# Kernel optimization log

Measured on AMD Instinct MI355X. Metric: run time of the kernel, lower is better.

## Reference

```python
import jax, jax.numpy as jnp
import numpy as np

B, N, C = 4, 2048, 1024
H = 16
D = C // H

def setup_inputs() -> dict:
    key = jax.random.key(0)
    k1, k2, k3 = jax.random.split(key, 3)
    x = jax.random.normal(k1, (B, N, C), dtype=jnp.float32)
    qkv_w = jax.random.normal(k2, (3 * C, C), dtype=jnp.float32) * (1.0 / np.sqrt(C))
    qkv_b = jax.random.normal(k3, (3 * C,), dtype=jnp.float32) * 0.02
    return {"x": x, "qkv_w": qkv_w, "qkv_b": qkv_b}

def reference(x, qkv_w, qkv_b):
    b, n, c = x.shape
    # torch Linear: x @ W^T + b
    qkv = x @ qkv_w.T + qkv_b                      # [B,N,3C]
    qkv = qkv.reshape(b, n, 3, H, D)
    qkv = jnp.transpose(qkv, (2, 0, 3, 1, 4))       # [3,B,H,N,D]
    q, k, v = qkv[0], qkv[1], qkv[2]
    attn = jnp.einsum('bhnd,bhmd->bhnm', q, k) / jnp.sqrt(jnp.asarray(D, x.dtype))
    attn = jax.nn.softmax(attn, axis=-1)
    out = jnp.einsum('bhnm,bhmd->bhnd', attn, v)    # [B,H,N,D]
    out = jnp.transpose(out, (0, 2, 1, 3)).reshape(b, n, c)
    return out
```

## Files before the change

### kernel.cpp

```cpp
#include <hip/hip_runtime.h>
#include <hip/hip_bf16.h>

typedef __attribute__((ext_vector_type(8))) short short8;
typedef __attribute__((ext_vector_type(4))) float f32x4;
typedef __attribute__((ext_vector_type(4))) unsigned int u32x4;
typedef unsigned short u16;
typedef unsigned int u32;

typedef u32 __attribute__((address_space(1))) as1_u32;
typedef u32 __attribute__((address_space(3))) as3_u32;

#define NB 4
#define SEQ 2048
#define CH 1024
#define NH 16
#define HD 64
#define M_TOT (NB*SEQ)
#define N_TOT (3*CH)
#define K_TOT CH
#define SCL 0.18033688f

#define MFMA16(a,b,c) __builtin_amdgcn_mfma_f32_16x16x32_bf16((a),(b),(c),0,0,0)

__device__ __forceinline__ u16 f2bf(float f) {
    union { float f; u32 u; } v; v.f = f;
    u32 u = v.u;
    return (u16)((u + 0x7fffu + ((u >> 16) & 1u)) >> 16);
}

__device__ __forceinline__ u32 pkbf2(float a, float b) {
    union { __hip_bfloat162 h; u32 u; } x;
    x.h = __float22bfloat162_rn(float2{a, b});
    return x.u;
}

__global__ void cvt_bf16_kernel(const float* __restrict__ x, u16* __restrict__ xb, int nx8,
                                const float* __restrict__ w, u16* __restrict__ wb, int nw8) {
    int i = blockIdx.x * 256 + threadIdx.x;
    const float* src; u16* dst; int idx;
    if (i < nx8) { src = x; dst = xb; idx = i; }
    else { idx = i - nx8; if (idx >= nw8) return; src = w; dst = wb; }
    const float4* s4 = (const float4*)src;
    float4 a = s4[2*idx], b = s4[2*idx+1];
    u32x4 r;
    r[0] = pkbf2(a.x, a.y); r[1] = pkbf2(a.z, a.w);
    r[2] = pkbf2(b.x, b.y); r[3] = pkbf2(b.z, b.w);
    *(u32x4*)(dst + (size_t)idx*8) = r;
}

__global__ __launch_bounds__(256) void qkv_gemm_kernel(
        const u16* __restrict__ A, const u16* __restrict__ W,
        const float* __restrict__ bias,
        u16* __restrict__ qw, u16* __restrict__ kw, u16* __restrict__ vtw)
{
    __shared__ u16 As[128*32];
    __shared__ u16 Bs[128*32];
    const int t = threadIdx.x;
    const int wave = t >> 6;
    const int lane = t & 63;
    const int l15 = lane & 15, lhi = lane >> 4;
    const int wr = wave >> 1, wc = wave & 1;
    const int xcd = blockIdx.x & 7;
    const int idx = blockIdx.x >> 3;
    const int bm = xcd * 8 + (idx & 7);
    const int bn = idx >> 3;

    f32x4 acc[4][4] = {};

    const int arow = t >> 2;
    const int acol = (t & 3) * 8;
    const u16* gA = A + (size_t)(bm*128 + arow)*K_TOT + acol;
    const u16* gB = W + (size_t)(bn*128 + arow)*K_TOT + acol;

    for (int k0 = 0; k0 < K_TOT; k0 += 32) {
        #pragma unroll
        for (int i = 0; i < 2; ++i) {
            __builtin_amdgcn_global_load_lds(
                (const as1_u32*)(gA + (size_t)i*64*K_TOT + k0),
                (as3_u32*)(As + i*2048 + wave*512), 16, 0, 0);
            __builtin_amdgcn_global_load_lds(
                (const as1_u32*)(gB + (size_t)i*64*K_TOT + k0),
                (as3_u32*)(Bs + i*2048 + wave*512), 16, 0, 0);
        }
        __syncthreads();
        short8 af[4], bfr[4];
        #pragma unroll
        for (int m = 0; m < 4; ++m)
            af[m] = *(const short8*)(As + (wr*64 + m*16 + l15)*32 + lhi*8);
        #pragma unroll
        for (int n = 0; n < 4; ++n)
            bfr[n] = *(const short8*)(Bs + (wc*64 + n*16 + l15)*32 + lhi*8);
        #pragma unroll
        for (int m = 0; m < 4; ++m)
            #pragma unroll
            for (int n = 0; n < 4; ++n)
                acc[m][n] = MFMA16(af[m], bfr[n], acc[m][n]);
        __syncthreads();
    }

    const int colbase = bn*128 + wc*64;
    const int which = colbase >> 10;
    float bv[4]; int hh[4], dd[4];
    #pragma unroll
    for (int n = 0; n < 4; ++n) {
        int cg = colbase + n*16 + l15;
        bv[n] = bias[cg];
        int hd = cg & 1023;
        hh[n] = hd >> 6; dd[n] = hd & 63;
    }
    #pragma unroll
    for (int m = 0; m < 4; ++m) {
        int rowg = bm*128 + wr*64 + m*16 + lhi*4;
        #pragma unroll
        for (int j = 0; j < 4; ++j) {
            int rg = rowg + j;
            int b = rg >> 11, nseq = rg & 2047;
            #pragma unroll
            for (int n = 0; n < 4; ++n) {
                float val = acc[m][n][j] + bv[n];
                size_t bhn = (size_t)(b*NH + hh[n]);
                if (which == 0) {
                    qw[(bhn*SEQ + nseq)*HD + dd[n]] = f2bf(val * SCL);
                } else if (which == 1) {
                    kw[(bhn*SEQ + nseq)*HD + dd[n]] = f2bf(val);
                } else {
                    vtw[(bhn*HD + dd[n])*SEQ + nseq] = f2bf(val);
                }
            }
        }
    }
}

__global__ __launch_bounds__(256, 2) void attn_kernel(
        const u16* __restrict__ qw, const u16* __restrict__ kw,
        const u16* __restrict__ vtw, float* __restrict__ out)
{
    __shared__ u16 Ksh[3][64*64];
    __shared__ u16 Vsh[3][64*64];
    const int t = threadIdx.x;
    const int wave = t >> 6, lane = t & 63;
    const int l15 = lane & 15, lhi = lane >> 4;
    const int bh = blockIdx.x & 63;
    const int b = bh >> 4, h = bh & 15;
    const int q0 = (blockIdx.x >> 6) * 256 + wave * 64;

    const u16* Q  = qw  + (size_t)bh * SEQ * HD;
    const u16* Kg = kw  + (size_t)bh * SEQ * HD;
    const u16* Vg = vtw + (size_t)bh * HD * SEQ;

    const int srow = lane >> 3;
    const int scol = ((lane & 7) ^ srow) * 8;

    auto STAGE = [&](int buf, int kv) {
        #pragma unroll
        for (int half = 0; half < 2; ++half) {
            int crow = wave*16 + half*8 + srow;
            int kperm = (crow & 32) | ((crow & 12) << 1)
                      | ((crow & 16) >> 2) | (crow & 3);
            __builtin_amdgcn_global_load_lds(
                (const as1_u32*)(Kg + (size_t)(kv + kperm)*HD + scol),
                (as3_u32*)(&Ksh[buf][(wave*16 + half*8)*64]), 16, 0, 0);
            __builtin_amdgcn_global_load_lds(
                (const as1_u32*)(Vg + (size_t)crow*SEQ + kv + scol),
                (as3_u32*)(&Vsh[buf][(wave*16 + half*8)*64]), 16, 0, 0);
        }
    };

    STAGE(0, 0);
    STAGE(1, 64);

    short8 qf[4][2];
    #pragma unroll
    for (int rf = 0; rf < 4; ++rf)
        #pragma unroll
        for (int ks = 0; ks < 2; ++ks)
            qf[rf][ks] = *(const short8*)(Q + (size_t)(q0 + rf*16 + l15)*HD + ks*32 + lhi*8);

    f32x4 o[4][4] = {};
    float lpart[4] = {0.f, 0.f, 0.f, 0.f};

    const int NT = SEQ / 64;
    int cur = 0;
    for (int tt = 0; tt < NT; ++tt) {
        asm volatile("s_waitcnt vmcnt(4)" ::: "memory");
        __builtin_amdgcn_s_barrier();
        __builtin_amdgcn_sched_barrier(0);

        int nxt = cur + 2; if (nxt >= 3) nxt -= 3;
        int kvn = (tt + 2 < NT) ? (tt + 2) * 64 : 0;
        STAGE(nxt, kvn);

        u32x4 pa[4];
        u32x4 pb[4];
        #pragma unroll
        for (int g = 0; g < 4; ++g) {
            f32x4 stg[4] = {};
            __builtin_amdgcn_s_setprio(1);
            #pragma unroll
            for (int ks = 0; ks < 2; ++ks) {
                short8 kf = *(const short8*)(&Ksh[cur][(g*16 + l15)*64 + ((ks*32 + lhi*8) ^ ((l15 & 7)*8))]);
                #pragma unroll
                for (int rf = 0; rf < 4; ++rf)
                    stg[rf] = MFMA16(kf, qf[rf][ks], stg[rf]);
            }
            __builtin_amdgcn_s_setprio(0);
            #pragma unroll
            for (int rf = 0; rf < 4; ++rf) {
                float p0 = __builtin_amdgcn_exp2f(stg[rf][0]);
                float p1 = __builtin_amdgcn_exp2f(stg[rf][1]);
                float p2 = __builtin_amdgcn_exp2f(stg[rf][2]);
                float p3 = __builtin_amdgcn_exp2f(stg[rf][3]);
                lpart[rf] += (p0 + p1) + (p2 + p3);
                if (g < 2) {
                    pa[rf][(g & 1)*2]     = pkbf2(p0, p1);
                    pa[rf][(g & 1)*2 + 1] = pkbf2(p2, p3);
                } else {
                    pb[rf][(g & 1)*2]     = pkbf2(p0, p1);
                    pb[rf][(g & 1)*2 + 1] = pkbf2(p2, p3);
                }
            }
        }

        __builtin_amdgcn_s_setprio(1);
        #pragma unroll
        for (int ks = 0; ks < 2; ++ks)
            #pragma unroll
            for (int nd = 0; nd < 4; ++nd) {
                short8 vf = *(const short8*)(&Vsh[cur][(nd*16 + l15)*64 + ((ks*32 + lhi*8) ^ ((l15 & 7)*8))]);
                #pragma unroll
                for (int rf = 0; rf < 4; ++rf) {
                    short8 pfrag = __builtin_bit_cast(short8, ks == 0 ? pa[rf] : pb[rf]);
                    o[rf][nd] = MFMA16(pfrag, vf, o[rf][nd]);
                }
            }
        __builtin_amdgcn_s_setprio(0);

        cur = cur + 1; if (cur >= 3) cur -= 3;
    }

    #pragma unroll
    for (int rf = 0; rf < 4; ++rf) {
        float l = lpart[rf];
        l += __shfl_xor(l, 16);
        l += __shfl_xor(l, 32);
        #pragma unroll
        for (int j = 0; j < 4; ++j) {
            float inv = 1.0f / __shfl(l, lhi*4 + j);
            int qrow = q0 + rf*16 + lhi*4 + j;
            float* orow = out + ((size_t)(b*SEQ + qrow))*CH + h*HD;
            #pragma unroll
            for (int nd = 0; nd < 4; ++nd)
                orow[nd*16 + l15] = o[rf][nd][j] * inv;
        }
    }
}

extern "C" void kernel_launch(void* const* d_in, const int* in_sizes, int n_in,
                              void* d_out, int out_size, void* d_ws, size_t ws_size,
                              hipStream_t stream) {
    const float* x    = (const float*)d_in[0];
    const float* w    = (const float*)d_in[1];
    const float* bias = (const float*)d_in[2];
    float* out = (float*)d_out;

    const size_t BHND = (size_t)NB*NH*SEQ*HD;
    u16* qw  = (u16*)d_ws;
    u16* kw  = qw  + BHND;
    u16* vtw = kw  + BHND;
    u16* xbf = vtw + BHND;
    u16* wbf = xbf + (size_t)M_TOT*K_TOT;

    const int nx8 = M_TOT*K_TOT/8;
    const int nw8 = N_TOT*K_TOT/8;
    cvt_bf16_kernel<<<(nx8+nw8+255)/256, 256, 0, stream>>>(x, xbf, nx8, w, wbf, nw8);
    qkv_gemm_kernel<<<(M_TOT/128)*(N_TOT/128), 256, 0, stream>>>(xbf, wbf, bias, qw, kw, vtw);
    attn_kernel<<<(SEQ/256)*NB*NH, 256, 0, stream>>>(qw, kw, vtw, out);
}
```

Baseline: 171.4 us.

## Triple-buffer QKV GEMM LDS tiles with async global_load_lds prefetch

The QKV projection GEMM now keeps three LDS stages for its A and B tiles and prefetches two k-tiles ahead using global_load_lds. A partial vmcnt wait plus a single barrier per iteration replaces the two __syncthreads per iteration, so global loads overlap the MFMA work. This triples LDS use for the GEMM, which may lower occupancy. At the end of the loop it issues redundant dummy loads of tile 0, which are wasted bandwidth.

```diff
diff --git a/kernel.cpp b/kernel.cpp
--- a/kernel.cpp
+++ b/kernel.cpp
@@ -53,8 +53,8 @@
         const float* __restrict__ bias,
         u16* __restrict__ qw, u16* __restrict__ kw, u16* __restrict__ vtw)
 {
-    __shared__ u16 As[128*32];
-    __shared__ u16 Bs[128*32];
+    __shared__ u16 As[3][128*32];
+    __shared__ u16 Bs[3][128*32];
     const int t = threadIdx.x;
     const int wave = t >> 6;
     const int lane = t & 63;
@@ -72,30 +72,46 @@
     const u16* gA = A + (size_t)(bm*128 + arow)*K_TOT + acol;
     const u16* gB = W + (size_t)(bn*128 + arow)*K_TOT + acol;
 
-    for (int k0 = 0; k0 < K_TOT; k0 += 32) {
+    auto STAGE = [&](int s, int kt) {
         #pragma unroll
         for (int i = 0; i < 2; ++i) {
             __builtin_amdgcn_global_load_lds(
-                (const as1_u32*)(gA + (size_t)i*64*K_TOT + k0),
-                (as3_u32*)(As + i*2048 + wave*512), 16, 0, 0);
-            __builtin_amdgcn_global_load_lds(
-                (const as1_u32*)(gB + (size_t)i*64*K_TOT + k0),
-                (as3_u32*)(Bs + i*2048 + wave*512), 16, 0, 0);
-        }
-        __syncthreads();
+                (const as1_u32*)(gA + (size_t)i*64*K_TOT + kt*32),
+                (as3_u32*)(As[s] + i*2048 + wave*512), 16, 0, 0);
+            __builtin_amdgcn_global_load_lds(
+                (const as1_u32*)(gB + (size_t)i*64*K_TOT + kt*32),
+                (as3_u32*)(Bs[s] + i*2048 + wave*512), 16, 0, 0);
+        }
+    };
+
+    STAGE(0, 0);
+    STAGE(1, 1);
+
+    const int NKT = K_TOT / 32;
+    int s = 0;
+    for (int kt = 0; kt < NKT; ++kt) {
+        asm volatile("s_waitcnt vmcnt(4)" ::: "memory");
+        __builtin_amdgcn_s_barrier();
+        __builtin_amdgcn_sched_barrier(0);
+
+        int s2 = (s + 2 >= 3) ? s - 1 : s + 2;
+        int ktn = (kt + 2 < NKT) ? kt + 2 : 0;
+        STAGE(s2, ktn);
+
         short8 af[4], bfr[4];
         #pragma unroll
         for (int m = 0; m < 4; ++m)
-            af[m] = *(const short8*)(As + (wr*64 + m*16 + l15)*32 + lhi*8);
+            af[m] = *(const short8*)(As[s] + (wr*64 + m*16 + l15)*32 + lhi*8);
         #pragma unroll
         for (int n = 0; n < 4; ++n)
-            bfr[n] = *(const short8*)(Bs + (wc*64 + n*16 + l15)*32 + lhi*8);
+            bfr[n] = *(const short8*)(Bs[s] + (wc*64 + n*16 + l15)*32 + lhi*8);
         #pragma unroll
         for (int m = 0; m < 4; ++m)
             #pragma unroll
             for (int n = 0; n < 4; ++n)
                 acc[m][n] = MFMA16(af[m], bfr[n], acc[m][n]);
-        __syncthreads();
+
+        s = (s + 1 >= 3) ? 0 : s + 1;
     }
 
     const int colbase = bn*128 + wc*64;
```

After: 170.0 us. About the same (-0.8%).

## Widen QKV GEMM K-tile to 64 with XOR-swizzled LDS layout

Applied to the files above, without the earlier changes.

The QKV projection GEMM now stages 64-wide K slices per iteration instead of 32, which halves the number of barrier pairs and loop iterations. The LDS tile is stored with an XOR swizzle of 16-byte groups by row, applied on the global source side of the direct-to-LDS loads, so that the MFMA fragment reads avoid bank conflicts. This doubles the LDS footprint per block and adds address arithmetic, and the kernel is still single-buffered.

```diff
diff --git a/kernel.cpp b/kernel.cpp
--- a/kernel.cpp
+++ b/kernel.cpp
@@ -53,8 +53,8 @@
         const float* __restrict__ bias,
         u16* __restrict__ qw, u16* __restrict__ kw, u16* __restrict__ vtw)
 {
-    __shared__ u16 As[128*32];
-    __shared__ u16 Bs[128*32];
+    __shared__ u16 As[128*64];
+    __shared__ u16 Bs[128*64];
     const int t = threadIdx.x;
     const int wave = t >> 6;
     const int lane = t & 63;
@@ -67,34 +67,49 @@
 
     f32x4 acc[4][4] = {};
 
-    const int arow = t >> 2;
-    const int acol = (t & 3) * 8;
-    const u16* gA = A + (size_t)(bm*128 + arow)*K_TOT + acol;
-    const u16* gB = W + (size_t)(bn*128 + arow)*K_TOT + acol;
-
-    for (int k0 = 0; k0 < K_TOT; k0 += 32) {
-        #pragma unroll
-        for (int i = 0; i < 2; ++i) {
-            __builtin_amdgcn_global_load_lds(
-                (const as1_u32*)(gA + (size_t)i*64*K_TOT + k0),
-                (as3_u32*)(As + i*2048 + wave*512), 16, 0, 0);
-            __builtin_amdgcn_global_load_lds(
-                (const as1_u32*)(gB + (size_t)i*64*K_TOT + k0),
-                (as3_u32*)(Bs + i*2048 + wave*512), 16, 0, 0);
+    const int srow = t >> 3;
+    const int sgr  = t & 7;
+
+    const u16* gA = A + (size_t)(bm*128)*K_TOT;
+    const u16* gB = W + (size_t)(bn*128)*K_TOT;
+
+    const int NKT = K_TOT / 64;
+    for (int kt = 0; kt < NKT; ++kt) {
+        #pragma unroll
+        for (int i = 0; i < 4; ++i) {
+            int row = i*32 + srow;
+            int gs = (sgr ^ (row & 7)) * 8;
+            __builtin_amdgcn_global_load_lds(
+                (const as1_u32*)(gA + (size_t)row*K_TOT + kt*64 + gs),
+                (as3_u32*)(As + row*64 + sgr*8), 16, 0, 0);
+            __builtin_amdgcn_global_load_lds(
+                (const as1_u32*)(gB + (size_t)row*K_TOT + kt*64 + gs),
+                (as3_u32*)(Bs + row*64 + sgr*8), 16, 0, 0);
         }
         __syncthreads();
-        short8 af[4], bfr[4];
+
+        short8 af[4][2], bfr[4][2];
+        #pragma unroll
+        for (int m = 0; m < 4; ++m) {
+            int row = wr*64 + m*16 + l15;
+            #pragma unroll
+            for (int kk = 0; kk < 2; ++kk)
+                af[m][kk] = *(const short8*)(&As[row*64 + (((kk*4 + lhi) ^ (row & 7))*8)]);
+        }
+        #pragma unroll
+        for (int n = 0; n < 4; ++n) {
+            int row = wc*64 + n*16 + l15;
+            #pragma unroll
+            for (int kk = 0; kk < 2; ++kk)
+                bfr[n][kk] = *(const short8*)(&Bs[row*64 + (((kk*4 + lhi) ^ (row & 7))*8)]);
+        }
         #pragma unroll
         for (int m = 0; m < 4; ++m)
-            af[m] = *(const short8*)(As + (wr*64 + m*16 + l15)*32 + lhi*8);
-        #pragma unroll
-        for (int n = 0; n < 4; ++n)
-            bfr[n] = *(const short8*)(Bs + (wc*64 + n*16 + l15)*32 + lhi*8);
-        #pragma unroll
-        for (int m = 0; m < 4; ++m)
-            #pragma unroll
-            for (int n = 0; n < 4; ++n)
-                acc[m][n] = MFMA16(af[m], bfr[n], acc[m][n]);
+            #pragma unroll
+            for (int n = 0; n < 4; ++n) {
+                acc[m][n] = MFMA16(af[m][0], bfr[n][0], acc[m][n]);
+                acc[m][n] = MFMA16(af[m][1], bfr[n][1], acc[m][n]);
+            }
         __syncthreads();
     }
 
```

Measured after the change: 166.2 us (median of 2 runs). 3.0% less time.
